# Optimization experiments

Measured on AMD Instinct MI355X. Metric: run time of the kernel, lower is better.

The kernel has to match this reference:

```python
import jax, jax.numpy as jnp
import numpy as np
import math

C, F, NH, W = 8, 256, 8, 1024  # channels, features (h), num_heads, frames (w)


def conv3x3(x, w):
    # x: [b,c,h,w], w: [out_c,in_c,3,3], padding=1, stride=1, no bias
    return jax.lax.conv_general_dilated(
        x, w, window_strides=(1, 1), padding=((1, 1), (1, 1)),
        dimension_numbers=("NCHW", "OIHW", "NCHW"))


def mc_linear_pw(x, w_pw):
    # per-channel linear over the feature (h) axis
    # x: [b,c,h,w], w_pw: [c, h_out, h_in] -> [b,c,h_out,w]
    return jnp.einsum("bchw,cgh->bcgw", x, w_pw)


def setup_inputs() -> dict:
    key = jax.random.key(0)
    ks = jax.random.split(key, 11)
    conv_s = 1.0 / math.sqrt(C * 9)
    pw_s = 1.0 / math.sqrt(F)
    dw_s = 1.0 / math.sqrt(C)
    return {
        "x": jax.random.normal(ks[0], (1, C, F, W), jnp.float32),
        "prev_qk": jax.random.normal(ks[1], (1, C, NH, W, W), jnp.float32),
        "wq_conv": jax.random.normal(ks[2], (C, C, 3, 3), jnp.float32) * conv_s,
        "wk_conv": jax.random.normal(ks[3], (C, C, 3, 3), jnp.float32) * conv_s,
        "wv_conv": jax.random.normal(ks[4], (C, C, 3, 3), jnp.float32) * conv_s,
        "wq_pw": jax.random.normal(ks[5], (C, F, F), jnp.float32) * pw_s,
        "wk_pw": jax.random.normal(ks[6], (C, F, F), jnp.float32) * pw_s,
        "wv_pw": jax.random.normal(ks[7], (C, F, F), jnp.float32) * pw_s,
        "wo_dw": jax.random.normal(ks[8], (C, C), jnp.float32) * dw_s,
        "wo_pw": jax.random.normal(ks[9], (C, F, F), jnp.float32) * pw_s,
    }


def reference(x, prev_qk, wq_conv, wk_conv, wv_conv, wq_pw, wk_pw, wv_pw, wo_dw, wo_pw):
    b, c, h, w = x.shape
    dh = h // NH

    def proj_heads(inp, w_conv, w_pw):
        p = mc_linear_pw(conv3x3(inp, w_conv), w_pw)          # [b,c,h,w]
        p = jnp.transpose(p, (0, 1, 3, 2))                     # [b,c,w,h]
        p = p.reshape(b, c, w, NH, dh)                         # [b,c,w,nh,dh]
        return jnp.transpose(p, (0, 1, 3, 2, 4))               # [b,c,nh,w,dh]

    q = proj_heads(x, wq_conv, wq_pw)
    k = proj_heads(x, wk_conv, wk_pw)
    v = proj_heads(x, wv_conv, wv_pw)

    # attention in fp32 over the frame (w) axis, scaled by sqrt(h) (features)
    qk = jnp.einsum("bcnqd,bcnkd->bcnqk", q.astype(jnp.float32), k.astype(jnp.float32)) / math.sqrt(h)
    qk = qk + prev_qk
    a = jnp.einsum("bcnqk,bcnkd->bcnqd", jax.nn.softmax(qk, axis=-1), v.astype(jnp.float32))
    a = jnp.transpose(a, (0, 1, 3, 2, 4)).reshape(b, c, w, h)  # [b,c,w,h]
    a = jnp.transpose(a, (0, 1, 3, 2))                          # [b,c,h,w]

    # o_proj: depthwise channel mix then per-channel positionwise linear
    o = jnp.einsum("bchw,dc->bdhw", a, wo_dw)
    out = mc_linear_pw(o, wo_pw)
    return (out, qk)
```

## Files before the change

### kernel.cpp

```cpp
#include <hip/hip_runtime.h>
#include <hip/hip_bf16.h>


typedef float f32x4 __attribute__((ext_vector_type(4)));
typedef short s16x8 __attribute__((ext_vector_type(8)));

static __device__ __forceinline__ unsigned short f2bf(float f) {
  unsigned int u = __builtin_bit_cast(unsigned int, f);
  u += 0x7fff + ((u >> 16) & 1);
  return (unsigned short)(u >> 16);
}

__global__ __launch_bounds__(256) void cvt_weights(
    const float* __restrict__ wq, const float* __restrict__ wk,
    const float* __restrict__ wv, const float* __restrict__ wo,
    unsigned short* __restrict__ dst) {
  int gid = blockIdx.x * 256 + threadIdx.x;
  int e = gid * 4;
  int arr = e >> 19;
  int off = e & 524287;
  const float* src = arr == 0 ? wq : arr == 1 ? wk : arr == 2 ? wv : wo;
  float4 v = *(const float4*)(src + off);
  ushort4 o;
  o.x = f2bf(v.x); o.y = f2bf(v.y); o.z = f2bf(v.z); o.w = f2bf(v.w);
  *(ushort4*)(dst + (size_t)arr * 524288 + off) = o;
}

__global__ __launch_bounds__(256) void conv3x3_k(
    const float* __restrict__ x,
    const float* __restrict__ wq, const float* __restrict__ wk,
    const float* __restrict__ wv,
    unsigned short* __restrict__ convT) {
  __shared__ float xt[8][34][36];
  int t = blockIdx.z;
  const float* wc = (t == 0) ? wq : (t == 1) ? wk : wv;
  int wtile = blockIdx.x * 32, htile = blockIdx.y * 32;
  int tid = threadIdx.x;
  for (int i = tid; i < 8 * 34 * 34; i += 256) {
    int cp = i / 1156;
    int rem = i - cp * 1156;
    int hh = rem / 34, ww = rem - hh * 34;
    int gh = htile + hh - 1, gw = wtile + ww - 1;
    float v = 0.f;
    if ((unsigned)gh < 256u && (unsigned)gw < 1024u)
      v = x[((size_t)cp * 256 + gh) * 1024 + gw];
    xt[cp][hh][ww] = v;
  }
  __syncthreads();
  int tx = tid & 31, strip = tid >> 5;
  int h0 = strip * 4;
  float acc[8][4];
#pragma unroll
  for (int co = 0; co < 8; ++co)
#pragma unroll
    for (int p = 0; p < 4; ++p) acc[co][p] = 0.f;
#pragma unroll 1
  for (int cp = 0; cp < 8; ++cp) {
    float xv[6][3];
#pragma unroll
    for (int rr = 0; rr < 6; ++rr)
#pragma unroll
      for (int cc = 0; cc < 3; ++cc)
        xv[rr][cc] = xt[cp][h0 + rr][tx + cc];
#pragma unroll
    for (int i = 0; i < 3; ++i)
#pragma unroll
      for (int j = 0; j < 3; ++j) {
#pragma unroll
        for (int co = 0; co < 8; ++co) {
          float wgt = wc[((co * 8 + cp) * 3 + i) * 3 + j];
#pragma unroll
          for (int p = 0; p < 4; ++p)
            acc[co][p] += wgt * xv[p + i][j];
        }
      }
  }
  int w = wtile + tx;
#pragma unroll
  for (int co = 0; co < 8; ++co) {
    ushort4 o;
    o.x = f2bf(acc[co][0]); o.y = f2bf(acc[co][1]);
    o.z = f2bf(acc[co][2]); o.w = f2bf(acc[co][3]);
    *(ushort4*)(convT + ((size_t)(t * 8 + co) * 1024 + w) * 256 + htile + h0) = o;
  }
}

__global__ __launch_bounds__(256) void gemm_pw(
    const unsigned short* __restrict__ A0,
    const unsigned short* __restrict__ B0,
    unsigned short* __restrict__ qkh,
    unsigned short* __restrict__ vstd,
    float* __restrict__ outp,
    int mode) {
  int b = blockIdx.z;
  const unsigned short* A = A0 + (size_t)b * 65536;
  const unsigned short* B = B0 + (size_t)b * 262144;
  int lane = threadIdx.x & 63, wvid = threadIdx.x >> 6;
  int wm = wvid & 1, wn = wvid >> 1;
  int mBase = blockIdx.y * 128 + wm * 64;
  int nBase = blockIdx.x * 128 + wn * 64;
  int c15 = lane & 15, klo = (lane >> 4) * 8;
  f32x4 acc[4][4];
#pragma unroll
  for (int mi = 0; mi < 4; ++mi)
#pragma unroll
    for (int ni = 0; ni < 4; ++ni) acc[mi][ni] = (f32x4){0.f, 0.f, 0.f, 0.f};
#pragma unroll 2
  for (int kk = 0; kk < 256; kk += 32) {
    s16x8 af[4], bf[4];
#pragma unroll
    for (int mi = 0; mi < 4; ++mi)
      af[mi] = *(const s16x8*)(A + (size_t)(mBase + mi * 16 + c15) * 256 + kk + klo);
#pragma unroll
    for (int ni = 0; ni < 4; ++ni)
      bf[ni] = *(const s16x8*)(B + (size_t)(nBase + ni * 16 + c15) * 256 + kk + klo);
#pragma unroll
    for (int mi = 0; mi < 4; ++mi)
#pragma unroll
      for (int ni = 0; ni < 4; ++ni)
        acc[mi][ni] = __builtin_amdgcn_mfma_f32_16x16x32_bf16(
            af[mi], bf[ni], acc[mi][ni], 0, 0, 0);
  }
  int r0 = (lane >> 4) * 4;
  if (mode == 0) {
    int t = b >> 3, c = b & 7;
    if (t < 2) {
      unsigned short* dst = qkh + (size_t)t * 2097152 + (size_t)c * 262144;
#pragma unroll
      for (int mi = 0; mi < 4; ++mi)
#pragma unroll
        for (int ni = 0; ni < 4; ++ni) {
          int g = mBase + mi * 16 + r0;
          int w = nBase + ni * 16 + c15;
          int n = g >> 5, d = g & 31;
          ushort4 o;
          o.x = f2bf(acc[mi][ni][0]); o.y = f2bf(acc[mi][ni][1]);
          o.z = f2bf(acc[mi][ni][2]); o.w = f2bf(acc[mi][ni][3]);
          *(ushort4*)(dst + ((size_t)n * 1024 + w) * 32 + d) = o;
        }
    } else {
      unsigned short* dst = vstd + (size_t)c * 262144;
#pragma unroll
      for (int mi = 0; mi < 4; ++mi)
#pragma unroll
        for (int ni = 0; ni < 4; ++ni) {
          int w = nBase + ni * 16 + c15;
#pragma unroll
          for (int r = 0; r < 4; ++r)
            dst[(size_t)(mBase + mi * 16 + r0 + r) * 1024 + w] = f2bf(acc[mi][ni][r]);
        }
    }
  } else {
    float* dst = outp + (size_t)b * 262144;
#pragma unroll
    for (int mi = 0; mi < 4; ++mi)
#pragma unroll
      for (int ni = 0; ni < 4; ++ni) {
        int w = nBase + ni * 16 + c15;
#pragma unroll
        for (int r = 0; r < 4; ++r)
          dst[(size_t)(mBase + mi * 16 + r0 + r) * 1024 + w] = acc[mi][ni][r];
      }
  }
}

__global__ __launch_bounds__(256) void attn_k(
    const unsigned short* __restrict__ Qh,
    const unsigned short* __restrict__ Kh,
    const unsigned short* __restrict__ Vstd,
    const float* __restrict__ prev,
    float* __restrict__ qkOut,
    float* __restrict__ aOut) {
  __shared__ unsigned short plds[4][16 * 80];
  int lane = threadIdx.x & 63, wvid = threadIdx.x >> 6;
  int cn = blockIdx.y;
  int c = cn >> 3, n = cn & 7;
  int qBase = blockIdx.x * 64 + wvid * 16;
  int c15 = lane & 15, quad = lane >> 4, klo = quad * 8;
  const unsigned short* Q = Qh + (size_t)cn * 32768;
  const unsigned short* K = Kh + (size_t)cn * 32768;
  const unsigned short* V = Vstd + (size_t)c * 262144 + (size_t)n * 32 * 1024;
  const float* prevB = prev + (size_t)cn * 1048576;
  float* qkB = qkOut + (size_t)cn * 1048576;
  s16x8 qf = *(const s16x8*)(Q + (size_t)(qBase + c15) * 32 + klo);
  f32x4 o0 = {0.f, 0.f, 0.f, 0.f}, o1 = {0.f, 0.f, 0.f, 0.f};
  float m[4], lsum[4];
#pragma unroll
  for (int r = 0; r < 4; ++r) { m[r] = -1e30f; lsum[r] = 0.f; }
  unsigned short* pw = plds[wvid];

  for (int kb = 0; kb < 1024; kb += 64) {
    float pv[4][4];
#pragma unroll
    for (int kt = 0; kt < 4; ++kt)
#pragma unroll
      for (int r = 0; r < 4; ++r) {
        int q = qBase + quad * 4 + r;
        pv[kt][r] = prevB[(size_t)q * 1024 + kb + kt * 16 + c15];
      }
    f32x4 s[4];
#pragma unroll
    for (int kt = 0; kt < 4; ++kt) {
      s16x8 kf = *(const s16x8*)(K + (size_t)(kb + kt * 16 + c15) * 32 + klo);
      f32x4 z = {0.f, 0.f, 0.f, 0.f};
      s[kt] = __builtin_amdgcn_mfma_f32_16x16x32_bf16(qf, kf, z, 0, 0, 0);
    }
#pragma unroll
    for (int kt = 0; kt < 4; ++kt)
#pragma unroll
      for (int r = 0; r < 4; ++r) {
        int q = qBase + quad * 4 + r;
        size_t idx = (size_t)q * 1024 + kb + kt * 16 + c15;
        float val = s[kt][r] * 0.0625f + pv[kt][r];
        s[kt][r] = val;
        qkB[idx] = val;
      }
    float cm[4], al[4], rs[4];
#pragma unroll
    for (int r = 0; r < 4; ++r)
      cm[r] = fmaxf(fmaxf(s[0][r], s[1][r]), fmaxf(s[2][r], s[3][r]));
#pragma unroll
    for (int d = 1; d < 16; d <<= 1)
#pragma unroll
      for (int r = 0; r < 4; ++r) cm[r] = fmaxf(cm[r], __shfl_xor(cm[r], d));
#pragma unroll
    for (int r = 0; r < 4; ++r) {
      float mn = fmaxf(m[r], cm[r]);
      al[r] = __expf(m[r] - mn);
      m[r] = mn;
      rs[r] = 0.f;
    }
#pragma unroll
    for (int kt = 0; kt < 4; ++kt)
#pragma unroll
      for (int r = 0; r < 4; ++r) {
        float p = __expf(s[kt][r] - m[r]);
        s[kt][r] = p;
        rs[r] += p;
      }
#pragma unroll
    for (int d = 1; d < 16; d <<= 1)
#pragma unroll
      for (int r = 0; r < 4; ++r) rs[r] += __shfl_xor(rs[r], d);
#pragma unroll
    for (int r = 0; r < 4; ++r) {
      lsum[r] = lsum[r] * al[r] + rs[r];
      o0[r] *= al[r];
      o1[r] *= al[r];
    }
#pragma unroll
    for (int kt = 0; kt < 4; ++kt)
#pragma unroll
      for (int r = 0; r < 4; ++r)
        pw[(quad * 4 + r) * 80 + kt * 16 + c15] = f2bf(s[kt][r]);
    __syncthreads();
#pragma unroll
    for (int kk2 = 0; kk2 < 2; ++kk2) {
      s16x8 pf = *(const s16x8*)(pw + c15 * 80 + kk2 * 32 + klo);
      s16x8 v0 = *(const s16x8*)(V + (size_t)c15 * 1024 + kb + kk2 * 32 + klo);
      s16x8 v1 = *(const s16x8*)(V + (size_t)(16 + c15) * 1024 + kb + kk2 * 32 + klo);
      o0 = __builtin_amdgcn_mfma_f32_16x16x32_bf16(pf, v0, o0, 0, 0, 0);
      o1 = __builtin_amdgcn_mfma_f32_16x16x32_bf16(pf, v1, o1, 0, 0, 0);
    }
  }
#pragma unroll
  for (int r = 0; r < 4; ++r) {
    float inv = 1.0f / lsum[r];
    int q = qBase + quad * 4 + r;
    aOut[((size_t)c * 256 + n * 32 + c15) * 1024 + q] = o0[r] * inv;
    aOut[((size_t)c * 256 + n * 32 + 16 + c15) * 1024 + q] = o1[r] * inv;
  }
}

__global__ __launch_bounds__(256) void mix_t(
    const float* __restrict__ a, const float* __restrict__ dw,
    unsigned short* __restrict__ ot) {
  int tx = threadIdx.x & 31, strip = threadIdx.x >> 5;
  int wtile = blockIdx.x * 32, htile = blockIdx.y * 32;
  int w = wtile + tx, h0 = htile + strip * 4;
  float acc[8][4];
#pragma unroll
  for (int co = 0; co < 8; ++co)
#pragma unroll
    for (int p = 0; p < 4; ++p) acc[co][p] = 0.f;
#pragma unroll 1
  for (int cp = 0; cp < 8; ++cp) {
    float av[4];
#pragma unroll
    for (int p = 0; p < 4; ++p)
      av[p] = a[((size_t)cp * 256 + h0 + p) * 1024 + w];
#pragma unroll
    for (int co = 0; co < 8; ++co) {
      float wgt = dw[co * 8 + cp];
#pragma unroll
      for (int p = 0; p < 4; ++p) acc[co][p] += wgt * av[p];
    }
  }
#pragma unroll
  for (int co = 0; co < 8; ++co) {
    ushort4 o;
    o.x = f2bf(acc[co][0]); o.y = f2bf(acc[co][1]);
    o.z = f2bf(acc[co][2]); o.w = f2bf(acc[co][3]);
    *(ushort4*)(ot + ((size_t)co * 1024 + w) * 256 + h0) = o;
  }
}

extern "C" void kernel_launch(void* const* d_in, const int* in_sizes, int n_in,
                              void* d_out, int out_size, void* d_ws, size_t ws_size,
                              hipStream_t stream) {
  (void)in_sizes; (void)n_in; (void)out_size; (void)ws_size;
  const float* x       = (const float*)d_in[0];
  const float* prev    = (const float*)d_in[1];
  const float* wq_conv = (const float*)d_in[2];
  const float* wk_conv = (const float*)d_in[3];
  const float* wv_conv = (const float*)d_in[4];
  const float* wq_pw   = (const float*)d_in[5];
  const float* wk_pw   = (const float*)d_in[6];
  const float* wv_pw   = (const float*)d_in[7];
  const float* wo_dw   = (const float*)d_in[8];
  const float* wo_pw   = (const float*)d_in[9];

  float* outp  = (float*)d_out;
  float* qkOut = outp + 2097152;

  char* ws = (char*)d_ws;
  unsigned short* pwB   = (unsigned short*)ws;
  unsigned short* convT = (unsigned short*)(ws + (4  << 20));
  unsigned short* qkh   = (unsigned short*)(ws + (16 << 20));
  unsigned short* vstd  = (unsigned short*)(ws + (24 << 20));
  float*          aBuf  = (float*)         (ws + (28 << 20));
  unsigned short* otB   = (unsigned short*)(ws + (36 << 20));

  cvt_weights<<<2048, 256, 0, stream>>>(wq_pw, wk_pw, wv_pw, wo_pw, pwB);
  conv3x3_k<<<dim3(32, 8, 3), 256, 0, stream>>>(x, wq_conv, wk_conv, wv_conv, convT);
  gemm_pw<<<dim3(8, 2, 24), 256, 0, stream>>>(pwB, convT, qkh, vstd, nullptr, 0);
  attn_k<<<dim3(16, 64), 256, 0, stream>>>(qkh, qkh + 2097152, vstd, prev, qkOut, aBuf);
  mix_t<<<dim3(32, 8), 256, 0, stream>>>(aBuf, wo_dw, otB);
  gemm_pw<<<dim3(8, 2, 8), 256, 0, stream>>>(pwB + 3 * 524288, otB, nullptr, nullptr, outp, 1);
}
```

Measured before the change: 578.7 us.

## Drop online max rescaling in attention softmax and prefetch next K/prev tiles

```diff
diff --git a/kernel.cpp b/kernel.cpp
--- a/kernel.cpp
+++ b/kernel.cpp
@@ -180,80 +180,51 @@
   const unsigned short* Q = Qh + (size_t)cn * 32768;
   const unsigned short* K = Kh + (size_t)cn * 32768;
   const unsigned short* V = Vstd + (size_t)c * 262144 + (size_t)n * 32 * 1024;
-  const float* prevB = prev + (size_t)cn * 1048576;
-  float* qkB = qkOut + (size_t)cn * 1048576;
+  const float* prevB = prev + (size_t)cn * 1048576 + (size_t)(qBase + quad * 4) * 1024 + c15;
+  float* qkB = qkOut + (size_t)cn * 1048576 + (size_t)(qBase + quad * 4) * 1024 + c15;
   s16x8 qf = *(const s16x8*)(Q + (size_t)(qBase + c15) * 32 + klo);
   f32x4 o0 = {0.f, 0.f, 0.f, 0.f}, o1 = {0.f, 0.f, 0.f, 0.f};
-  float m[4], lsum[4];
-#pragma unroll
-  for (int r = 0; r < 4; ++r) { m[r] = -1e30f; lsum[r] = 0.f; }
+  float lsum[4] = {0.f, 0.f, 0.f, 0.f};
   unsigned short* pw = plds[wvid];
 
+  float pvA[4][4];
+  s16x8 kfA[4];
+#pragma unroll
+  for (int kt = 0; kt < 4; ++kt) {
+    kfA[kt] = *(const s16x8*)(K + (size_t)(kt * 16 + c15) * 32 + klo);
+#pragma unroll
+    for (int r = 0; r < 4; ++r)
+      pvA[kt][r] = prevB[(size_t)r * 1024 + kt * 16];
+  }
+
+#pragma unroll 1
   for (int kb = 0; kb < 1024; kb += 64) {
-    float pv[4][4];
+    int kbn = (kb + 64) & 1023;
+    f32x4 s[4];
+#pragma unroll
+    for (int kt = 0; kt < 4; ++kt) {
+      f32x4 z = {0.f, 0.f, 0.f, 0.f};
+      s[kt] = __builtin_amdgcn_mfma_f32_16x16x32_bf16(qf, kfA[kt], z, 0, 0, 0);
+    }
+    float pvN[4][4];
+    s16x8 kfN[4];
+#pragma unroll
+    for (int kt = 0; kt < 4; ++kt) {
+      kfN[kt] = *(const s16x8*)(K + (size_t)(kbn + kt * 16 + c15) * 32 + klo);
+#pragma unroll
+      for (int r = 0; r < 4; ++r)
+        pvN[kt][r] = prevB[(size_t)r * 1024 + kbn + kt * 16];
+    }
 #pragma unroll
     for (int kt = 0; kt < 4; ++kt)
 #pragma unroll
       for (int r = 0; r < 4; ++r) {
-        int q = qBase + quad * 4 + r;
-        pv[kt][r] = prevB[(size_t)q * 1024 + kb + kt * 16 + c15];
+        float val = s[kt][r] * 0.0625f + pvA[kt][r];
+        qkB[(size_t)r * 1024 + kb + kt * 16] = val;
+        float p = __expf(val);
+        lsum[r] += p;
+        pw[(quad * 4 + r) * 80 + kt * 16 + c15] = f2bf(p);
       }
-    f32x4 s[4];
-#pragma unroll
-    for (int kt = 0; kt < 4; ++kt) {
-      s16x8 kf = *(const s16x8*)(K + (size_t)(kb + kt * 16 + c15) * 32 + klo);
-      f32x4 z = {0.f, 0.f, 0.f, 0.f};
-      s[kt] = __builtin_amdgcn_mfma_f32_16x16x32_bf16(qf, kf, z, 0, 0, 0);
-    }
-#pragma unroll
-    for (int kt = 0; kt < 4; ++kt)
-#pragma unroll
-      for (int r = 0; r < 4; ++r) {
-        int q = qBase + quad * 4 + r;
-        size_t idx = (size_t)q * 1024 + kb + kt * 16 + c15;
-        float val = s[kt][r] * 0.0625f + pv[kt][r];
-        s[kt][r] = val;
-        qkB[idx] = val;
-      }
-    float cm[4], al[4], rs[4];
-#pragma unroll
-    for (int r = 0; r < 4; ++r)
-      cm[r] = fmaxf(fmaxf(s[0][r], s[1][r]), fmaxf(s[2][r], s[3][r]));
-#pragma unroll
-    for (int d = 1; d < 16; d <<= 1)
-#pragma unroll
-      for (int r = 0; r < 4; ++r) cm[r] = fmaxf(cm[r], __shfl_xor(cm[r], d));
-#pragma unroll
-    for (int r = 0; r < 4; ++r) {
-      float mn = fmaxf(m[r], cm[r]);
-      al[r] = __expf(m[r] - mn);
-      m[r] = mn;
-      rs[r] = 0.f;
-    }
-#pragma unroll
-    for (int kt = 0; kt < 4; ++kt)
-#pragma unroll
-      for (int r = 0; r < 4; ++r) {
-        float p = __expf(s[kt][r] - m[r]);
-        s[kt][r] = p;
-        rs[r] += p;
-      }
-#pragma unroll
-    for (int d = 1; d < 16; d <<= 1)
-#pragma unroll
-      for (int r = 0; r < 4; ++r) rs[r] += __shfl_xor(rs[r], d);
-#pragma unroll
-    for (int r = 0; r < 4; ++r) {
-      lsum[r] = lsum[r] * al[r] + rs[r];
-      o0[r] *= al[r];
-      o1[r] *= al[r];
-    }
-#pragma unroll
-    for (int kt = 0; kt < 4; ++kt)
-#pragma unroll
-      for (int r = 0; r < 4; ++r)
-        pw[(quad * 4 + r) * 80 + kt * 16 + c15] = f2bf(s[kt][r]);
-    __syncthreads();
 #pragma unroll
     for (int kk2 = 0; kk2 < 2; ++kk2) {
       s16x8 pf = *(const s16x8*)(pw + c15 * 80 + kk2 * 32 + klo);
@@ -262,7 +233,17 @@
       o0 = __builtin_amdgcn_mfma_f32_16x16x32_bf16(pf, v0, o0, 0, 0, 0);
       o1 = __builtin_amdgcn_mfma_f32_16x16x32_bf16(pf, v1, o1, 0, 0, 0);
     }
-  }
+#pragma unroll
+    for (int kt = 0; kt < 4; ++kt) {
+      kfA[kt] = kfN[kt];
+#pragma unroll
+      for (int r = 0; r < 4; ++r) pvA[kt][r] = pvN[kt][r];
+    }
+  }
+#pragma unroll
+  for (int d = 1; d < 16; d <<= 1)
+#pragma unroll
+    for (int r = 0; r < 4; ++r) lsum[r] += __shfl_xor(lsum[r], d);
 #pragma unroll
   for (int r = 0; r < 4; ++r) {
     float inv = 1.0f / lsum[r];
```

After: 575.7 us. Within noise of the previous version (-0.5%).
